# Kernel tuning notes

Measured on AMD Instinct MI355X. Metric: run time of the kernel, lower is better.

Reference implementation:

```python
import jax, jax.numpy as jnp
import numpy as np

PALACE_N = 64   # base palace mask size
PALACE_BLOCK = 8  # 8 palaces of 8 positions each


def _palace_base():
    # base 64x64 mask: 1.0 within a palace (8x8 diagonal blocks), 0.5 across palaces
    pid = jnp.arange(PALACE_N) // PALACE_BLOCK
    intra = pid[:, None] == pid[None, :]
    return jnp.where(intra, 1.0, 0.5).astype(jnp.float32)


def _get_mask(T, inter_palace_weight):
    # tile base mask by index modulo 64 (matches mask[i % 64, j % 64])
    base = _palace_base()
    ii = jnp.arange(T) % PALACE_N
    base_T = base[ii[:, None], ii[None, :]]            # [T, T]
    intra = (base_T == 1.0).astype(jnp.float32)
    inter = (base_T < 1.0).astype(jnp.float32)
    return intra + jax.nn.sigmoid(inter_palace_weight) * inter


def setup_inputs() -> dict:
    key = jax.random.key(0)
    ks = jax.random.split(key, 5)
    B, T, D = 4, 2048, 1024
    x = jax.random.normal(ks[0], (B, T, D), dtype=jnp.float32)
    s = 1.0 / np.sqrt(D)
    Wq = jax.random.normal(ks[1], (D, D), dtype=jnp.float32) * s
    Wk = jax.random.normal(ks[2], (D, D), dtype=jnp.float32) * s
    Wv = jax.random.normal(ks[3], (D, D), dtype=jnp.float32) * s
    inter_palace_weight = jnp.float32(0.1)
    return {"x": x, "Wq": Wq, "Wk": Wk, "Wv": Wv,
            "inter_palace_weight": inter_palace_weight}


def reference(x, Wq, Wk, Wv, inter_palace_weight):
    B, T, D = x.shape
    H = 16
    hd = D // H
    scale = hd ** -0.5
    pmask = _get_mask(T, inter_palace_weight)          # [T, T]
    # torch Linear: x @ W.T
    q = (x @ Wq.T).reshape(B, T, H, hd)
    k = (x @ Wk.T).reshape(B, T, H, hd)
    v = (x @ Wv.T).reshape(B, T, H, hd)
    attn = jnp.einsum('bqhd,bkhd->bhqk', q, k) * scale
    attn = attn * pmask[None, None, :, :]
    attn = jax.nn.softmax(attn, axis=-1)
    attn = jnp.nan_to_num(attn, nan=0.0)
    out = jnp.einsum('bhqk,bkhd->bqhd', attn, v)
    return out.reshape(B, T, D)
```

## Files before the change

kernel.cpp:

```cpp
#include <hip/hip_runtime.h>

typedef unsigned short u16;
typedef unsigned int u32;
typedef short bf16x8 __attribute__((ext_vector_type(8)));
typedef float f32x4 __attribute__((ext_vector_type(4)));
typedef u32 u32x4 __attribute__((ext_vector_type(4)));

#define AS_GLOBAL __attribute__((address_space(1)))
#define AS_LDS __attribute__((address_space(3)))

__device__ __forceinline__ void async16(const void* g, void* l) {
  __builtin_amdgcn_global_load_lds((const AS_GLOBAL u32*)g, (AS_LDS u32*)l, 16, 0, 0);
}

__device__ __forceinline__ u16 f2bf(float f) {
  u32 u = __builtin_bit_cast(u32, f);
  u += 0x7FFFu + ((u >> 16) & 1u);
  return (u16)(u >> 16);
}

__device__ __forceinline__ u32 pk2bf(float lo, float hi) {
  return __builtin_amdgcn_perm(__builtin_bit_cast(u32, hi),
                               __builtin_bit_cast(u32, lo), 0x07060302u);
}

__device__ __forceinline__ float fexp2(float x) {
#if __has_builtin(__builtin_amdgcn_exp2f)
  return __builtin_amdgcn_exp2f(x);
#else
  return exp2f(x);
#endif
}

__global__ __launch_bounds__(256) void cvt_all(const float* __restrict__ x,
                                               const float* __restrict__ wq,
                                               const float* __restrict__ wk,
                                               const float* __restrict__ wv,
                                               u16* __restrict__ xb,
                                               u16* __restrict__ wb) {
  const int blk = blockIdx.x;
  const float* src;
  u16* dst;
  int i;
  if (blk < 8192) {
    src = x; dst = xb; i = blk * 256 + threadIdx.x;
  } else if (blk < 9216) {
    src = wq; dst = wb; i = (blk - 8192) * 256 + threadIdx.x;
  } else if (blk < 10240) {
    src = wk; dst = wb + 1048576; i = (blk - 9216) * 256 + threadIdx.x;
  } else {
    src = wv; dst = wb + 2097152; i = (blk - 10240) * 256 + threadIdx.x;
  }
  float4 f = reinterpret_cast<const float4*>(src)[i];
  ushort4 o;
  o.x = f2bf(f.x); o.y = f2bf(f.y); o.z = f2bf(f.z); o.w = f2bf(f.w);
  reinterpret_cast<ushort4*>(dst)[i] = o;
}

__global__ __launch_bounds__(256, 2) void qkv_gemm(const u16* __restrict__ X,
                                                   const u16* __restrict__ W,
                                                   u16* __restrict__ O) {
  const int z = blockIdx.z;
  const u16* Wz = W + (size_t)z * (1024 * 1024);
  u16* Oz = O + (size_t)z * (8192 * 1024);

  __shared__ __align__(16) u16 SMEM[4][8192];

  const int t = threadIdx.x;
  const int lane = t & 63, w = t >> 6, quad = lane >> 4, lq = lane & 15;
  const int wm = (w >> 1) * 64, wn = (w & 1) * 64;
  const int sw = lq & 7;
  const size_t m0 = (size_t)blockIdx.x * 128;
  const int n0 = blockIdx.y * 128;

  int off[4];
#pragma unroll
  for (int j = 0; j < 4; ++j) {
    const int s = j * 256 + t, row = s >> 3, c = (s & 7) ^ (row & 7);
    off[j] = row * 1024 + c * 8;
  }
  const u16* gA = X + m0 * 1024;
  const u16* gB = Wz + (size_t)n0 * 1024;

  f32x4 acc[4][4];
#pragma unroll
  for (int i = 0; i < 4; ++i)
#pragma unroll
    for (int j = 0; j < 4; ++j) acc[i][j] = f32x4{0.f, 0.f, 0.f, 0.f};

  auto stage = [&](int kt, int nb) {
    const u16* ga = gA + kt * 64;
    const u16* gb = gB + kt * 64;
#pragma unroll
    for (int j = 0; j < 4; ++j)
      async16(ga + off[j], &SMEM[nb][(j * 256 + t) * 8]);
#pragma unroll
    for (int j = 0; j < 4; ++j)
      async16(gb + off[j], &SMEM[2 + nb][(j * 256 + t) * 8]);
  };

  stage(0, 0);

  for (int kt = 0; kt < 16; ++kt) {
    const int cur = kt & 1;
    __syncthreads();
    if (kt < 15) stage(kt + 1, cur ^ 1);

    bf16x8 Af[4][2], Bf[4][2];
#pragma unroll
    for (int i = 0; i < 4; ++i)
#pragma unroll
      for (int ks = 0; ks < 2; ++ks) {
        Af[i][ks] = *reinterpret_cast<const bf16x8*>(
            &SMEM[cur][(wm + i * 16 + lq) * 64 + ((ks * 4 + quad) ^ sw) * 8]);
        Bf[i][ks] = *reinterpret_cast<const bf16x8*>(
            &SMEM[2 + cur][(wn + i * 16 + lq) * 64 + ((ks * 4 + quad) ^ sw) * 8]);
      }
#pragma unroll
    for (int i = 0; i < 4; ++i)
#pragma unroll
      for (int j = 0; j < 4; ++j) {
        acc[i][j] = __builtin_amdgcn_mfma_f32_16x16x32_bf16(Af[i][0], Bf[j][0], acc[i][j], 0, 0, 0);
        acc[i][j] = __builtin_amdgcn_mfma_f32_16x16x32_bf16(Af[i][1], Bf[j][1], acc[i][j], 0, 0, 0);
      }
  }

  __syncthreads();
  u16* ep = &SMEM[w][0];
  if (z != 2) {
#pragma unroll
    for (int i = 0; i < 4; ++i)
#pragma unroll
      for (int j = 0; j < 4; ++j)
#pragma unroll
        for (int r = 0; r < 4; ++r)
          ep[(i * 16 + quad * 4 + r) * 80 + j * 16 + lq] = f2bf(acc[i][j][r]);
  } else {
#pragma unroll
    for (int i = 0; i < 4; ++i)
#pragma unroll
      for (int j = 0; j < 4; ++j)
#pragma unroll
        for (int r = 0; r < 4; ++r)
          ep[(j * 16 + lq) * 80 + i * 16 + quad * 4 + r] = f2bf(acc[i][j][r]);
  }
  asm volatile("s_waitcnt lgkmcnt(0)" ::: "memory");

  const int r8 = lane >> 3, c8 = lane & 7;
  const size_t ms = m0 + wm;
  const size_t bb = ms >> 11, tt0 = ms & 2047;
  const int hh = (n0 + wn) >> 6;
  if (z != 2) {
    u16* gbase = Oz + ((bb * 16 + hh) * 2048 + tt0) * 64;
#pragma unroll
    for (int kq = 0; kq < 8; ++kq) {
      const int row = kq * 8 + r8;
      bf16x8 v = *reinterpret_cast<const bf16x8*>(&ep[row * 80 + c8 * 8]);
      *reinterpret_cast<bf16x8*>(&gbase[(size_t)row * 64 + c8 * 8]) = v;
    }
  } else {
    u16* gbase = Oz + ((size_t)(bb * 16 + hh) * 64) * 2048 + tt0;
#pragma unroll
    for (int kq = 0; kq < 8; ++kq) {
      const int row = kq * 8 + r8;
      bf16x8 v = *reinterpret_cast<const bf16x8*>(&ep[row * 80 + c8 * 8]);
      *reinterpret_cast<bf16x8*>(&gbase[(size_t)row * 2048 + c8 * 8]) = v;
    }
  }
}

__global__ __launch_bounds__(512, 4) void palace_attn(const u16* __restrict__ Q,
                                                      const u16* __restrict__ K,
                                                      const u16* __restrict__ Vt,
                                                      float* __restrict__ out,
                                                      const float* __restrict__ wptr) {
  const int bh = blockIdx.x, qt = blockIdx.y;
  const int h = bh & 15, b = bh >> 4;
  const size_t base = (size_t)bh * (2048 * 64);

  __shared__ __align__(16) u16 Ks[2][64 * 64];
  __shared__ __align__(16) u16 Vs[2][64 * 64];

  const int t = threadIdx.x;
  const int w = t >> 6, lane = t & 63, quad = lane >> 4, lq = lane & 15;
  const int lq3 = lq >> 3;
  const int swk = (lq & 3) | (((lq >> 2) & 1) << 2);
  const int swv = (lq & 3) | (lq3 << 2);
  const float sig = 1.f / (1.f + __expf(-wptr[0]));
  const float Ci = 0.125f * 1.44269504f;
  const float Co = Ci * sig;
  const float MC = 14.4269504f;

  const int qs0 = (w & 1) * 4;
  float cft[2][2];
#pragma unroll
  for (int half = 0; half < 2; ++half)
#pragma unroll
    for (int qg = 0; qg < 2; ++qg)
      cft[half][qg] = (half * 4 + quad == qs0 + qg * 2 + lq3) ? Ci : Co;

  bf16x8 qf[2][2];
#pragma unroll
  for (int qg = 0; qg < 2; ++qg)
#pragma unroll
    for (int kc = 0; kc < 2; ++kc)
      qf[qg][kc] = *reinterpret_cast<const bf16x8*>(
          Q + base + (size_t)(qt * 256 + w * 32 + qg * 16 + lq) * 64 + kc * 32 + quad * 8);

  const int row_s = t >> 3;
  const int sr_s = (row_s & 3) | (((row_s >> 3) & 1) << 2);
  const int cl_s = (t & 7) ^ sr_s;
  const int ko = row_s * 64 + cl_s * 8;
  const int vo = row_s * 2048 + cl_s * 8;

  f32x4 O[2][4];
  f32x4 Lacc[2];
#pragma unroll
  for (int qg = 0; qg < 2; ++qg) {
    Lacc[qg] = f32x4{0.f, 0.f, 0.f, 0.f};
#pragma unroll
    for (int dg = 0; dg < 4; ++dg) O[qg][dg] = f32x4{0.f, 0.f, 0.f, 0.f};
  }

  const short oneb = (short)0x3F80;
  const bf16x8 ones8 = {oneb, oneb, oneb, oneb, oneb, oneb, oneb, oneb};

  const int h0 = w & 1;

  {
    const u16* kgp = K + base;
    const u16* vgp = Vt + base;
    async16(kgp + ko, &Ks[0][(w * 64) * 8]);
    async16(vgp + vo, &Vs[0][(w * 64) * 8]);
  }

  for (int kt = 0; kt < 32; ++kt) {
    const int cur = kt & 1;
    __syncthreads();
    if (kt < 31) {
      const u16* kgp = K + base + (size_t)(kt + 1) * 4096;
      const u16* vgp = Vt + base + (size_t)(kt + 1) * 64;
      const int nb = cur ^ 1;
      async16(kgp + ko, &Ks[nb][(w * 64) * 8]);
      async16(vgp + vo, &Vs[nb][(w * 64) * 8]);
    }

#pragma unroll
    for (int hx = 0; hx < 2; ++hx) {
      const int half = hx ^ h0;
      const int rb = half * 32 + ((lq >> 2) << 3) + (lq & 3);
      bf16x8 kf[2][2];
#pragma unroll
      for (int kg2 = 0; kg2 < 2; ++kg2) {
        const int krow = rb + kg2 * 4;
        kf[kg2][0] = *reinterpret_cast<const bf16x8*>(
            &Ks[cur][krow * 64 + (quad ^ swk) * 8]);
        kf[kg2][1] = *reinterpret_cast<const bf16x8*>(
            &Ks[cur][krow * 64 + ((quad + 4) ^ swk) * 8]);
      }

      bf16x8 vbf[4];
#pragma unroll
      for (int dg = 0; dg < 4; ++dg)
        vbf[dg] = *reinterpret_cast<const bf16x8*>(
            &Vs[cur][(dg * 16 + lq) * 64 + ((half * 4 + quad) ^ swv) * 8]);

#pragma unroll
      for (int qg = 0; qg < 2; ++qg) {
        f32x4 z0 = {0.f, 0.f, 0.f, 0.f}, z1 = {0.f, 0.f, 0.f, 0.f};
        __builtin_amdgcn_s_setprio(1);
        z0 = __builtin_amdgcn_mfma_f32_16x16x32_bf16(kf[0][0], qf[qg][0], z0, 0, 0, 0);
        z0 = __builtin_amdgcn_mfma_f32_16x16x32_bf16(kf[0][1], qf[qg][1], z0, 0, 0, 0);
        z1 = __builtin_amdgcn_mfma_f32_16x16x32_bf16(kf[1][0], qf[qg][0], z1, 0, 0, 0);
        z1 = __builtin_amdgcn_mfma_f32_16x16x32_bf16(kf[1][1], qf[qg][1], z1, 0, 0, 0);
        __builtin_amdgcn_s_setprio(0);

        const float cf = cft[half][qg];
        const float p0 = fexp2(__builtin_fmaf(z0[0], cf, -MC));
        const float p1 = fexp2(__builtin_fmaf(z0[1], cf, -MC));
        const float p2 = fexp2(__builtin_fmaf(z0[2], cf, -MC));
        const float p3 = fexp2(__builtin_fmaf(z0[3], cf, -MC));
        const float p4 = fexp2(__builtin_fmaf(z1[0], cf, -MC));
        const float p5 = fexp2(__builtin_fmaf(z1[1], cf, -MC));
        const float p6 = fexp2(__builtin_fmaf(z1[2], cf, -MC));
        const float p7 = fexp2(__builtin_fmaf(z1[3], cf, -MC));

        u32x4 pk;
        pk.x = pk2bf(p0, p1);
        pk.y = pk2bf(p2, p3);
        pk.z = pk2bf(p4, p5);
        pk.w = pk2bf(p6, p7);
        const bf16x8 pa = __builtin_bit_cast(bf16x8, pk);

        __builtin_amdgcn_s_setprio(1);
        Lacc[qg] = __builtin_amdgcn_mfma_f32_16x16x32_bf16(pa, ones8, Lacc[qg], 0, 0, 0);
#pragma unroll
        for (int dg = 0; dg < 4; ++dg)
          O[qg][dg] = __builtin_amdgcn_mfma_f32_16x16x32_bf16(pa, vbf[dg], O[qg][dg], 0, 0, 0);
        __builtin_amdgcn_s_setprio(0);
      }
    }
  }

#pragma unroll
  for (int qg = 0; qg < 2; ++qg) {
#pragma unroll
    for (int r = 0; r < 4; ++r) {
      const float iv = 1.f / Lacc[qg][r];
      const size_t trow = (size_t)(qt * 256 + w * 32 + qg * 16 + quad * 4 + r);
      float* op = out + ((size_t)b * 2048 + trow) * 1024 + h * 64 + lq;
#pragma unroll
      for (int dg = 0; dg < 4; ++dg) op[dg * 16] = O[qg][dg][r] * iv;
    }
  }
}

extern "C" void kernel_launch(void* const* d_in, const int* in_sizes, int n_in,
                              void* d_out, int out_size, void* d_ws, size_t ws_size,
                              hipStream_t stream) {
  (void)in_sizes; (void)n_in; (void)out_size; (void)ws_size;
  const float* x = (const float*)d_in[0];
  const float* Wq = (const float*)d_in[1];
  const float* Wk = (const float*)d_in[2];
  const float* Wv = (const float*)d_in[3];
  const float* wip = (const float*)d_in[4];
  float* out = (float*)d_out;

  u16* xb = (u16*)d_ws;
  u16* wb = xb + 8388608;
  u16* qb = wb + 3145728;
  u16* kb = qb + 8388608;
  u16* vb = kb + 8388608;

  cvt_all<<<11264, 256, 0, stream>>>(x, Wq, Wk, Wv, xb, wb);
  qkv_gemm<<<dim3(64, 8, 3), 256, 0, stream>>>(xb, wb, qb);
  palace_attn<<<dim3(64, 8, 1), 512, 0, stream>>>(qb, kb, vb, out, wip);
}
```

Baseline: 212.1 us.

## Use 8-wave GEMM blocks and 128-key attention tiles to halve barriers

The QKV GEMM now runs 512 threads per block, with each wave computing a 64x32 sub-tile instead of 64x64. This lowers accumulator register pressure and raises occupancy, and the epilogue staging is adjusted to match. The attention kernel now stages 128 keys per iteration instead of 64, which halves the number of loop iterations and __syncthreads barriers. In exchange it doubles LDS use per block, which may limit occupancy, and it relies on reusing the palace-coefficient lookup via half&1, which is valid because the palace period of 64 divides the tile.

```diff
diff --git a/kernel.cpp b/kernel.cpp
--- a/kernel.cpp
+++ b/kernel.cpp
@@ -57,7 +57,7 @@
   reinterpret_cast<ushort4*>(dst)[i] = o;
 }
 
-__global__ __launch_bounds__(256, 2) void qkv_gemm(const u16* __restrict__ X,
+__global__ __launch_bounds__(512, 4) void qkv_gemm(const u16* __restrict__ X,
                                                    const u16* __restrict__ W,
                                                    u16* __restrict__ O) {
   const int z = blockIdx.z;
@@ -68,35 +68,35 @@
 
   const int t = threadIdx.x;
   const int lane = t & 63, w = t >> 6, quad = lane >> 4, lq = lane & 15;
-  const int wm = (w >> 1) * 64, wn = (w & 1) * 64;
+  const int wm = (w >> 2) * 64, wn = (w & 3) * 32;
   const int sw = lq & 7;
   const size_t m0 = (size_t)blockIdx.x * 128;
   const int n0 = blockIdx.y * 128;
 
-  int off[4];
-#pragma unroll
-  for (int j = 0; j < 4; ++j) {
-    const int s = j * 256 + t, row = s >> 3, c = (s & 7) ^ (row & 7);
+  int off[2];
+#pragma unroll
+  for (int j = 0; j < 2; ++j) {
+    const int s = j * 512 + t, row = s >> 3, c = (s & 7) ^ (row & 7);
     off[j] = row * 1024 + c * 8;
   }
   const u16* gA = X + m0 * 1024;
   const u16* gB = Wz + (size_t)n0 * 1024;
 
-  f32x4 acc[4][4];
+  f32x4 acc[4][2];
 #pragma unroll
   for (int i = 0; i < 4; ++i)
 #pragma unroll
-    for (int j = 0; j < 4; ++j) acc[i][j] = f32x4{0.f, 0.f, 0.f, 0.f};
+    for (int j = 0; j < 2; ++j) acc[i][j] = f32x4{0.f, 0.f, 0.f, 0.f};
 
   auto stage = [&](int kt, int nb) {
     const u16* ga = gA + kt * 64;
     const u16* gb = gB + kt * 64;
 #pragma unroll
-    for (int j = 0; j < 4; ++j)
-      async16(ga + off[j], &SMEM[nb][(j * 256 + t) * 8]);
-#pragma unroll
-    for (int j = 0; j < 4; ++j)
-      async16(gb + off[j], &SMEM[2 + nb][(j * 256 + t) * 8]);
+    for (int j = 0; j < 2; ++j)
+      async16(ga + off[j], &SMEM[nb][(j * 512 + t) * 8]);
+#pragma unroll
+    for (int j = 0; j < 2; ++j)
+      async16(gb + off[j], &SMEM[2 + nb][(j * 512 + t) * 8]);
   };
 
   stage(0, 0);
@@ -106,65 +106,63 @@
     __syncthreads();
     if (kt < 15) stage(kt + 1, cur ^ 1);
 
-    bf16x8 Af[4][2], Bf[4][2];
-#pragma unroll
-    for (int i = 0; i < 4; ++i)
-#pragma unroll
-      for (int ks = 0; ks < 2; ++ks) {
+    bf16x8 Af[4][2], Bf[2][2];
+#pragma unroll
+    for (int ks = 0; ks < 2; ++ks) {
+#pragma unroll
+      for (int i = 0; i < 4; ++i)
         Af[i][ks] = *reinterpret_cast<const bf16x8*>(
             &SMEM[cur][(wm + i * 16 + lq) * 64 + ((ks * 4 + quad) ^ sw) * 8]);
-        Bf[i][ks] = *reinterpret_cast<const bf16x8*>(
-            &SMEM[2 + cur][(wn + i * 16 + lq) * 64 + ((ks * 4 + quad) ^ sw) * 8]);
-      }
+#pragma unroll
+      for (int j = 0; j < 2; ++j)
+        Bf[j][ks] = *reinterpret_cast<const bf16x8*>(
+            &SMEM[2 + cur][(wn + j * 16 + lq) * 64 + ((ks * 4 + quad) ^ sw) * 8]);
+    }
 #pragma unroll
     for (int i = 0; i < 4; ++i)
 #pragma unroll
-      for (int j = 0; j < 4; ++j) {
+      for (int j = 0; j < 2; ++j) {
         acc[i][j] = __builtin_amdgcn_mfma_f32_16x16x32_bf16(Af[i][0], Bf[j][0], acc[i][j], 0, 0, 0);
         acc[i][j] = __builtin_amdgcn_mfma_f32_16x16x32_bf16(Af[i][1], Bf[j][1], acc[i][j], 0, 0, 0);
       }
   }
 
   __syncthreads();
-  u16* ep = &SMEM[w][0];
-  if (z != 2) {
-#pragma unroll
-    for (int i = 0; i < 4; ++i)
-#pragma unroll
-      for (int j = 0; j < 4; ++j)
-#pragma unroll
-        for (int r = 0; r < 4; ++r)
-          ep[(i * 16 + quad * 4 + r) * 80 + j * 16 + lq] = f2bf(acc[i][j][r]);
-  } else {
-#pragma unroll
-    for (int i = 0; i < 4; ++i)
-#pragma unroll
-      for (int j = 0; j < 4; ++j)
-#pragma unroll
-        for (int r = 0; r < 4; ++r)
-          ep[(j * 16 + lq) * 80 + i * 16 + quad * 4 + r] = f2bf(acc[i][j][r]);
-  }
-  asm volatile("s_waitcnt lgkmcnt(0)" ::: "memory");
-
-  const int r8 = lane >> 3, c8 = lane & 7;
+  u16* ep = &SMEM[0][0] + w * 2560;
   const size_t ms = m0 + wm;
   const size_t bb = ms >> 11, tt0 = ms & 2047;
-  const int hh = (n0 + wn) >> 6;
+  const int hh = (n0 + wn) >> 6, d0 = (n0 + wn) & 63;
   if (z != 2) {
-    u16* gbase = Oz + ((bb * 16 + hh) * 2048 + tt0) * 64;
-#pragma unroll
-    for (int kq = 0; kq < 8; ++kq) {
-      const int row = kq * 8 + r8;
-      bf16x8 v = *reinterpret_cast<const bf16x8*>(&ep[row * 80 + c8 * 8]);
-      *reinterpret_cast<bf16x8*>(&gbase[(size_t)row * 64 + c8 * 8]) = v;
+#pragma unroll
+    for (int i = 0; i < 4; ++i)
+#pragma unroll
+      for (int j = 0; j < 2; ++j)
+#pragma unroll
+        for (int r = 0; r < 4; ++r)
+          ep[(i * 16 + quad * 4 + r) * 36 + j * 16 + lq] = f2bf(acc[i][j][r]);
+    asm volatile("s_waitcnt lgkmcnt(0)" ::: "memory");
+    u16* gbase = Oz + ((bb * 16 + hh) * 2048 + tt0) * 64 + d0;
+#pragma unroll
+    for (int kq = 0; kq < 4; ++kq) {
+      const int row = kq * 16 + (lane >> 2), c = lane & 3;
+      bf16x8 v = *reinterpret_cast<const bf16x8*>(&ep[row * 36 + c * 8]);
+      *reinterpret_cast<bf16x8*>(&gbase[(size_t)row * 64 + c * 8]) = v;
     }
   } else {
-    u16* gbase = Oz + ((size_t)(bb * 16 + hh) * 64) * 2048 + tt0;
-#pragma unroll
-    for (int kq = 0; kq < 8; ++kq) {
-      const int row = kq * 8 + r8;
-      bf16x8 v = *reinterpret_cast<const bf16x8*>(&ep[row * 80 + c8 * 8]);
-      *reinterpret_cast<bf16x8*>(&gbase[(size_t)row * 2048 + c8 * 8]) = v;
+#pragma unroll
+    for (int i = 0; i < 4; ++i)
+#pragma unroll
+      for (int j = 0; j < 2; ++j)
+#pragma unroll
+        for (int r = 0; r < 4; ++r)
+          ep[(j * 16 + lq) * 72 + i * 16 + quad * 4 + r] = f2bf(acc[i][j][r]);
+    asm volatile("s_waitcnt lgkmcnt(0)" ::: "memory");
+    u16* gbase = Oz + ((size_t)(bb * 16 + hh) * 64 + d0) * 2048 + tt0;
+#pragma unroll
+    for (int kq = 0; kq < 4; ++kq) {
+      const int row = kq * 8 + (lane >> 3), c = lane & 7;
+      bf16x8 v = *reinterpret_cast<const bf16x8*>(&ep[row * 72 + c * 8]);
+      *reinterpret_cast<bf16x8*>(&gbase[(size_t)row * 2048 + c * 8]) = v;
     }
   }
 }
@@ -178,8 +176,8 @@
   const int h = bh & 15, b = bh >> 4;
   const size_t base = (size_t)bh * (2048 * 64);
 
-  __shared__ __align__(16) u16 Ks[2][64 * 64];
-  __shared__ __align__(16) u16 Vs[2][64 * 64];
+  __shared__ __align__(16) u16 Ks[2][128 * 64];
+  __shared__ __align__(16) u16 Vs[2][64 * 128];
 
   const int t = threadIdx.x;
   const int w = t >> 6, lane = t & 63, quad = lane >> 4, lq = lane & 15;
@@ -194,10 +192,10 @@
   const int qs0 = (w & 1) * 4;
   float cft[2][2];
 #pragma unroll
-  for (int half = 0; half < 2; ++half)
+  for (int hb = 0; hb < 2; ++hb)
 #pragma unroll
     for (int qg = 0; qg < 2; ++qg)
-      cft[half][qg] = (half * 4 + quad == qs0 + qg * 2 + lq3) ? Ci : Co;
+      cft[hb][qg] = (hb * 4 + quad == qs0 + qg * 2 + lq3) ? Ci : Co;
 
   bf16x8 qf[2][2];
 #pragma unroll
@@ -207,11 +205,17 @@
       qf[qg][kc] = *reinterpret_cast<const bf16x8*>(
           Q + base + (size_t)(qt * 256 + w * 32 + qg * 16 + lq) * 64 + kc * 32 + quad * 8);
 
-  const int row_s = t >> 3;
-  const int sr_s = (row_s & 3) | (((row_s >> 3) & 1) << 2);
-  const int cl_s = (t & 7) ^ sr_s;
-  const int ko = row_s * 64 + cl_s * 8;
-  const int vo = row_s * 2048 + cl_s * 8;
+  int ko[2], vo[2];
+#pragma unroll
+  for (int r = 0; r < 2; ++r) {
+    const int s = r * 512 + t;
+    const int rk = s >> 3;
+    const int srk = (rk & 3) | (((rk >> 3) & 1) << 2);
+    ko[r] = rk * 64 + ((s & 7) ^ srk) * 8;
+    const int rv = s >> 4;
+    const int srv = (rv & 3) | (((rv >> 3) & 1) << 2);
+    vo[r] = rv * 2048 + ((s & 15) ^ srv) * 8;
+  }
 
   f32x4 O[2][4];
   f32x4 Lacc[2];
@@ -225,29 +229,29 @@
   const short oneb = (short)0x3F80;
   const bf16x8 ones8 = {oneb, oneb, oneb, oneb, oneb, oneb, oneb, oneb};
 
-  const int h0 = w & 1;
-
-  {
-    const u16* kgp = K + base;
-    const u16* vgp = Vt + base;
-    async16(kgp + ko, &Ks[0][(w * 64) * 8]);
-    async16(vgp + vo, &Vs[0][(w * 64) * 8]);
-  }
-
-  for (int kt = 0; kt < 32; ++kt) {
+  const int h0 = w & 3;
+
+  auto stage = [&](int kt, int nb) {
+    const u16* kgp = K + base + (size_t)kt * 8192;
+    const u16* vgp = Vt + base + (size_t)kt * 128;
+#pragma unroll
+    for (int r = 0; r < 2; ++r) {
+      async16(kgp + ko[r], &Ks[nb][(r * 512 + t) * 8]);
+      async16(vgp + vo[r], &Vs[nb][(r * 512 + t) * 8]);
+    }
+  };
+
+  stage(0, 0);
+
+  for (int kt = 0; kt < 16; ++kt) {
     const int cur = kt & 1;
     __syncthreads();
-    if (kt < 31) {
-      const u16* kgp = K + base + (size_t)(kt + 1) * 4096;
-      const u16* vgp = Vt + base + (size_t)(kt + 1) * 64;
-      const int nb = cur ^ 1;
-      async16(kgp + ko, &Ks[nb][(w * 64) * 8]);
-      async16(vgp + vo, &Vs[nb][(w * 64) * 8]);
-    }
-
-#pragma unroll
-    for (int hx = 0; hx < 2; ++hx) {
+    if (kt < 15) stage(kt + 1, cur ^ 1);
+
+#pragma unroll
+    for (int hx = 0; hx < 4; ++hx) {
       const int half = hx ^ h0;
+      const int hb = half & 1;
       const int rb = half * 32 + ((lq >> 2) << 3) + (lq & 3);
       bf16x8 kf[2][2];
 #pragma unroll
@@ -263,7 +267,7 @@
 #pragma unroll
       for (int dg = 0; dg < 4; ++dg)
         vbf[dg] = *reinterpret_cast<const bf16x8*>(
-            &Vs[cur][(dg * 16 + lq) * 64 + ((half * 4 + quad) ^ swv) * 8]);
+            &Vs[cur][(dg * 16 + lq) * 128 + ((half * 4 + quad) ^ swv) * 8]);
 
 #pragma unroll
       for (int qg = 0; qg < 2; ++qg) {
@@ -275,7 +279,7 @@
         z1 = __builtin_amdgcn_mfma_f32_16x16x32_bf16(kf[1][1], qf[qg][1], z1, 0, 0, 0);
         __builtin_amdgcn_s_setprio(0);
 
-        const float cf = cft[half][qg];
+        const float cf = cft[hb][qg];
         const float p0 = fexp2(__builtin_fmaf(z0[0], cf, -MC));
         const float p1 = fexp2(__builtin_fmaf(z0[1], cf, -MC));
         const float p2 = fexp2(__builtin_fmaf(z0[2], cf, -MC));
@@ -333,6 +337,6 @@
   u16* vb = kb + 8388608;
 
   cvt_all<<<11264, 256, 0, stream>>>(x, Wq, Wk, Wv, xb, wb);
-  qkv_gemm<<<dim3(64, 8, 3), 256, 0, stream>>>(xb, wb, qb);
+  qkv_gemm<<<dim3(64, 8, 3), 512, 0, stream>>>(xb, wb, qb);
   palace_attn<<<dim3(64, 8, 1), 512, 0, stream>>>(qb, kb, vb, out, wip);
 }
```

Result: no change. 212.1 us (+0.0%).
